# Performance work log

Hardware: AMD Instinct MI355X
Metric: run time of the kernel (lower is better)

## Reference

```python
import jax, jax.numpy as jnp
import numpy as np


def setup_inputs() -> dict:
    key = jax.random.key(0)
    k1, k2 = jax.random.split(key)
    _p = jax.random.normal(k1, (8192, 4096), dtype=jnp.float32)
    _q = jax.random.normal(k2, (8192, 4096), dtype=jnp.float32)
    return {"_p": _p, "_q": _q}


def reference(_p, _q):
    # softmax over class dim (dim 1)
    p = jax.nn.softmax(_p, axis=1)
    q = jax.nn.softmax(_q, axis=1)
    m = 0.5 * (p + q)
    # elementwise Jensen-Shannon divergence contribution per entry
    jsd = 0.5 * (q * jnp.log(q / m) + p * jnp.log(p / m))
    # weighted Euclidean: sum over rows of sqrt(sum_j (dp^2 * jsd))
    d2 = jnp.square(_p - _q)
    weuc = jnp.sum(jnp.sqrt(jnp.sum(d2 * jsd, axis=1)))
    return weuc
```

## Files before the change

### kernel.cpp

```cpp
#include <hip/hip_runtime.h>
#include <math.h>

constexpr int ROWS = 8192;
constexpr int COLS = 4096;
constexpr int TPB  = 256;
constexpr int WAVES = TPB / 64;
constexpr int EPT  = COLS / TPB;

__device__ __forceinline__ float wave_sum(float v) {
    #pragma unroll
    for (int o = 32; o > 0; o >>= 1) v += __shfl_xor(v, o, 64);
    return v;
}

__device__ __forceinline__ float wave_max(float v) {
    #pragma unroll
    for (int o = 32; o > 0; o >>= 1) v = fmaxf(v, __shfl_xor(v, o, 64));
    return v;
}

__device__ __forceinline__ float block_sum(float v, float* smem, int tid) {
    v = wave_sum(v);
    const int wid = tid >> 6, lane = tid & 63;
    if (lane == 0) smem[wid] = v;
    __syncthreads();
    if (wid == 0) {
        float x = (lane < WAVES) ? smem[lane] : 0.0f;
        x = wave_sum(x);
        if (lane == 0) smem[0] = x;
    }
    __syncthreads();
    const float r = smem[0];
    __syncthreads();
    return r;
}

__device__ __forceinline__ float block_max(float v, float* smem, int tid) {
    v = wave_max(v);
    const int wid = tid >> 6, lane = tid & 63;
    if (lane == 0) smem[wid] = v;
    __syncthreads();
    if (wid == 0) {
        float x = (lane < WAVES) ? smem[lane] : -INFINITY;
        x = wave_max(x);
        if (lane == 0) smem[0] = x;
    }
    __syncthreads();
    const float r = smem[0];
    __syncthreads();
    return r;
}

__global__ __launch_bounds__(TPB) void wjs_row_kernel(const float* __restrict__ P,
                                                      const float* __restrict__ Q,
                                                      float* __restrict__ rowres) {
    __shared__ float smem[WAVES];
    const int row = blockIdx.x;
    const int tid = threadIdx.x;
    const float* __restrict__ prow = P + (size_t)row * COLS;
    const float* __restrict__ qrow = Q + (size_t)row * COLS;

    float vp[EPT], vq[EPT];
    #pragma unroll
    for (int c = 0; c < EPT / 4; ++c) {
        const int col = c * (TPB * 4) + tid * 4;
        const float4 a = *reinterpret_cast<const float4*>(prow + col);
        const float4 b = *reinterpret_cast<const float4*>(qrow + col);
        vp[4*c+0] = a.x; vp[4*c+1] = a.y; vp[4*c+2] = a.z; vp[4*c+3] = a.w;
        vq[4*c+0] = b.x; vq[4*c+1] = b.y; vq[4*c+2] = b.z; vq[4*c+3] = b.w;
    }

    float mp = -INFINITY, mq = -INFINITY;
    #pragma unroll
    for (int i = 0; i < EPT; ++i) { mp = fmaxf(mp, vp[i]); mq = fmaxf(mq, vq[i]); }
    mp = block_max(mp, smem, tid);
    mq = block_max(mq, smem, tid);

    float ep[EPT], eq[EPT];
    float sp = 0.0f, sq = 0.0f;
    #pragma unroll
    for (int i = 0; i < EPT; ++i) {
        ep[i] = __expf(vp[i] - mp); sp += ep[i];
        eq[i] = __expf(vq[i] - mq); sq += eq[i];
    }
    sp = block_sum(sp, smem, tid);
    sq = block_sum(sq, smem, tid);

    const float inv_sp = 1.0f / sp;
    const float inv_sq = 1.0f / sq;
    const float lsp = __logf(sp);
    const float lsq = __logf(sq);

    float acc = 0.0f;
    #pragma unroll
    for (int i = 0; i < EPT; ++i) {
        const float p  = ep[i] * inv_sp;
        const float q  = eq[i] * inv_sq;
        const float m  = 0.5f * (p + q);
        const float lm = __logf(m);
        const float lp = (vp[i] - mp) - lsp;
        const float lq = (vq[i] - mq) - lsq;
        const float jsd = 0.5f * (q * (lq - lm) + p * (lp - lm));
        const float d  = vp[i] - vq[i];
        acc = fmaf(d * d, jsd, acc);
    }
    acc = block_sum(acc, smem, tid);
    if (tid == 0) rowres[row] = sqrtf(fmaxf(acc, 0.0f));
}

__global__ __launch_bounds__(TPB) void wjs_final_kernel(const float* __restrict__ rowres,
                                                        float* __restrict__ out) {
    __shared__ float smem[WAVES];
    float acc = 0.0f;
    for (int i = threadIdx.x; i < ROWS; i += TPB) acc += rowres[i];
    acc = block_sum(acc, smem, threadIdx.x);
    if (threadIdx.x == 0) out[0] = acc;
}

extern "C" void kernel_launch(void* const* d_in, const int* in_sizes, int n_in,
                              void* d_out, int out_size, void* d_ws, size_t ws_size,
                              hipStream_t stream) {
    const float* P = (const float*)d_in[0];
    const float* Q = (const float*)d_in[1];
    float* rowres  = (float*)d_ws;
    float* out     = (float*)d_out;

    wjs_row_kernel<<<ROWS, TPB, 0, stream>>>(P, Q, rowres);
    wjs_final_kernel<<<1, TPB, 0, stream>>>(rowres, out);
}
```

Baseline: 286.5 us.

## Map one row per wavefront to drop block-level reductions and barriers

```diff
diff --git a/kernel.cpp b/kernel.cpp
--- a/kernel.cpp
+++ b/kernel.cpp
@@ -1,11 +1,11 @@
 #include <hip/hip_runtime.h>
 #include <math.h>
 
-constexpr int ROWS = 8192;
-constexpr int COLS = 4096;
-constexpr int TPB  = 256;
-constexpr int WAVES = TPB / 64;
-constexpr int EPT  = COLS / TPB;
+constexpr int ROWS   = 8192;
+constexpr int COLS   = 4096;
+constexpr int TPB    = 256;
+constexpr int WPB    = TPB / 64;
+constexpr int CHUNKS = COLS / (64 * 4);
 
 __device__ __forceinline__ float wave_sum(float v) {
     #pragma unroll
@@ -13,78 +13,45 @@
     return v;
 }
 
-__device__ __forceinline__ float wave_max(float v) {
+__global__ __launch_bounds__(TPB, 3) void wjs_row_kernel(const float* __restrict__ P,
+                                                         const float* __restrict__ Q,
+                                                         float* __restrict__ rowres) {
+    const int lane = threadIdx.x & 63;
+    const int wid  = threadIdx.x >> 6;
+    const int row  = blockIdx.x * WPB + wid;
+
+    const float4* __restrict__ p4 = reinterpret_cast<const float4*>(P + (size_t)row * COLS);
+    const float4* __restrict__ q4 = reinterpret_cast<const float4*>(Q + (size_t)row * COLS);
+
+    float4 vp[CHUNKS], vq[CHUNKS];
     #pragma unroll
-    for (int o = 32; o > 0; o >>= 1) v = fmaxf(v, __shfl_xor(v, o, 64));
-    return v;
-}
-
-__device__ __forceinline__ float block_sum(float v, float* smem, int tid) {
-    v = wave_sum(v);
-    const int wid = tid >> 6, lane = tid & 63;
-    if (lane == 0) smem[wid] = v;
-    __syncthreads();
-    if (wid == 0) {
-        float x = (lane < WAVES) ? smem[lane] : 0.0f;
-        x = wave_sum(x);
-        if (lane == 0) smem[0] = x;
-    }
-    __syncthreads();
-    const float r = smem[0];
-    __syncthreads();
-    return r;
-}
-
-__device__ __forceinline__ float block_max(float v, float* smem, int tid) {
-    v = wave_max(v);
-    const int wid = tid >> 6, lane = tid & 63;
-    if (lane == 0) smem[wid] = v;
-    __syncthreads();
-    if (wid == 0) {
-        float x = (lane < WAVES) ? smem[lane] : -INFINITY;
-        x = wave_max(x);
-        if (lane == 0) smem[0] = x;
-    }
-    __syncthreads();
-    const float r = smem[0];
-    __syncthreads();
-    return r;
-}
-
-__global__ __launch_bounds__(TPB) void wjs_row_kernel(const float* __restrict__ P,
-                                                      const float* __restrict__ Q,
-                                                      float* __restrict__ rowres) {
-    __shared__ float smem[WAVES];
-    const int row = blockIdx.x;
-    const int tid = threadIdx.x;
-    const float* __restrict__ prow = P + (size_t)row * COLS;
-    const float* __restrict__ qrow = Q + (size_t)row * COLS;
-
-    float vp[EPT], vq[EPT];
-    #pragma unroll
-    for (int c = 0; c < EPT / 4; ++c) {
-        const int col = c * (TPB * 4) + tid * 4;
-        const float4 a = *reinterpret_cast<const float4*>(prow + col);
-        const float4 b = *reinterpret_cast<const float4*>(qrow + col);
-        vp[4*c+0] = a.x; vp[4*c+1] = a.y; vp[4*c+2] = a.z; vp[4*c+3] = a.w;
-        vq[4*c+0] = b.x; vq[4*c+1] = b.y; vq[4*c+2] = b.z; vq[4*c+3] = b.w;
+    for (int c = 0; c < CHUNKS; ++c) {
+        vp[c] = p4[c * 64 + lane];
+        vq[c] = q4[c * 64 + lane];
     }
 
     float mp = -INFINITY, mq = -INFINITY;
     #pragma unroll
-    for (int i = 0; i < EPT; ++i) { mp = fmaxf(mp, vp[i]); mq = fmaxf(mq, vq[i]); }
-    mp = block_max(mp, smem, tid);
-    mq = block_max(mq, smem, tid);
+    for (int c = 0; c < CHUNKS; ++c) {
+        mp = fmaxf(mp, fmaxf(fmaxf(vp[c].x, vp[c].y), fmaxf(vp[c].z, vp[c].w)));
+        mq = fmaxf(mq, fmaxf(fmaxf(vq[c].x, vq[c].y), fmaxf(vq[c].z, vq[c].w)));
+    }
+    #pragma unroll
+    for (int o = 32; o > 0; o >>= 1) {
+        mp = fmaxf(mp, __shfl_xor(mp, o, 64));
+        mq = fmaxf(mq, __shfl_xor(mq, o, 64));
+    }
 
-    float ep[EPT], eq[EPT];
     float sp = 0.0f, sq = 0.0f;
     #pragma unroll
-    for (int i = 0; i < EPT; ++i) {
-        ep[i] = __expf(vp[i] - mp); sp += ep[i];
-        eq[i] = __expf(vq[i] - mq); sq += eq[i];
+    for (int c = 0; c < CHUNKS; ++c) {
+        sp += __expf(vp[c].x - mp) + __expf(vp[c].y - mp)
+            + __expf(vp[c].z - mp) + __expf(vp[c].w - mp);
+        sq += __expf(vq[c].x - mq) + __expf(vq[c].y - mq)
+            + __expf(vq[c].z - mq) + __expf(vq[c].w - mq);
     }
-    sp = block_sum(sp, smem, tid);
-    sq = block_sum(sq, smem, tid);
+    sp = wave_sum(sp);
+    sq = wave_sum(sq);
 
     const float inv_sp = 1.0f / sp;
     const float inv_sq = 1.0f / sq;
@@ -93,28 +60,45 @@
 
     float acc = 0.0f;
     #pragma unroll
-    for (int i = 0; i < EPT; ++i) {
-        const float p  = ep[i] * inv_sp;
-        const float q  = eq[i] * inv_sq;
-        const float m  = 0.5f * (p + q);
-        const float lm = __logf(m);
-        const float lp = (vp[i] - mp) - lsp;
-        const float lq = (vq[i] - mq) - lsq;
-        const float jsd = 0.5f * (q * (lq - lm) + p * (lp - lm));
-        const float d  = vp[i] - vq[i];
-        acc = fmaf(d * d, jsd, acc);
+    for (int c = 0; c < CHUNKS; ++c) {
+        const float xps[4] = {vp[c].x, vp[c].y, vp[c].z, vp[c].w};
+        const float xqs[4] = {vq[c].x, vq[c].y, vq[c].z, vq[c].w};
+        #pragma unroll
+        for (int k = 0; k < 4; ++k) {
+            const float tp = xps[k] - mp;
+            const float tq = xqs[k] - mq;
+            const float p  = __expf(tp) * inv_sp;
+            const float q  = __expf(tq) * inv_sq;
+            const float m  = 0.5f * (p + q);
+            const float lm = __logf(m);
+            const float lp = tp - lsp;
+            const float lq = tq - lsq;
+            const float jsd = 0.5f * (q * (lq - lm) + p * (lp - lm));
+            const float d = xps[k] - xqs[k];
+            acc = fmaf(d * d, jsd, acc);
+        }
     }
-    acc = block_sum(acc, smem, tid);
-    if (tid == 0) rowres[row] = sqrtf(fmaxf(acc, 0.0f));
+    acc = wave_sum(acc);
+    if (lane == 0)
+        rowres[row] = sqrtf(fmaxf(acc, 0.0f));
+
 }
 
-__global__ __launch_bounds__(TPB) void wjs_final_kernel(const float* __restrict__ rowres,
-                                                        float* __restrict__ out) {
-    __shared__ float smem[WAVES];
+__global__ __launch_bounds__(1024) void wjs_final_kernel(const float* __restrict__ rowres,
+                                                         float* __restrict__ out) {
+    __shared__ float smem[16];
+    const int tid = threadIdx.x;
     float acc = 0.0f;
-    for (int i = threadIdx.x; i < ROWS; i += TPB) acc += rowres[i];
-    acc = block_sum(acc, smem, threadIdx.x);
-    if (threadIdx.x == 0) out[0] = acc;
+    for (int i = tid; i < ROWS; i += 1024) acc += rowres[i];
+    acc = wave_sum(acc);
+    const int wid = tid >> 6, lane = tid & 63;
+    if (lane == 0) smem[wid] = acc;
+    __syncthreads();
+    if (wid == 0) {
+        float x = (lane < 16) ? smem[lane] : 0.0f;
+        x = wave_sum(x);
+        if (lane == 0) out[0] = x;
+    }
 }
 
 extern "C" void kernel_launch(void* const* d_in, const int* in_sizes, int n_in,
@@ -125,6 +109,6 @@
     float* rowres  = (float*)d_ws;
     float* out     = (float*)d_out;
 
-    wjs_row_kernel<<<ROWS, TPB, 0, stream>>>(P, Q, rowres);
-    wjs_final_kernel<<<1, TPB, 0, stream>>>(rowres, out);
+    wjs_row_kernel<<<ROWS / WPB, TPB, 0, stream>>>(P, Q, rowres);
+    wjs_final_kernel<<<1, 1024, 0, stream>>>(rowres, out);
 }
```

New measurement: 448.7 us. 56.6% more time.
